# Optimization experiments

Measured on AMD Instinct MI355X. Metric: run time of the kernel, lower is better.

The kernel has to match this reference:

```python
import jax, jax.numpy as jnp
import numpy as np

K = 20
EPS = 1e-5
NEG_SLOPE = 0.2


def _graph_feature(x, k):
    # x: [B, N, C] -> edge features [B, N, k, 2C]
    xx = jnp.sum(x * x, axis=-1)                       # [B, N]
    inner = jnp.einsum('bnc,bmc->bnm', x, x)           # [B, N, N]
    neg_dist = 2.0 * inner - xx[:, :, None] - xx[:, None, :]
    idx = jax.lax.top_k(neg_dist, k)[1]                # [B, N, k] nearest neighbors
    nbr = jax.vmap(lambda f, i: f[i])(x, idx)          # [B, N, k, C]
    center = jnp.broadcast_to(x[:, :, None, :], nbr.shape)
    return jnp.concatenate([nbr - center, center], axis=-1)


def _bn(y, gamma, beta, axes):
    mu = y.mean(axes, keepdims=True)
    var = y.var(axes, keepdims=True)
    return (y - mu) * jax.lax.rsqrt(var + EPS) * gamma + beta


def _lrelu(y):
    return jnp.where(y > 0, y, NEG_SLOPE * y)


def _edge_block(feat, w, gamma, beta):
    # feat: [B, N, k, Cin], w: [Cout, Cin] (1x1 conv)
    y = jnp.einsum('bnkc,oc->bnko', feat, w)
    y = _lrelu(_bn(y, gamma, beta, (0, 1, 2)))
    return y.max(axis=2)                               # max over k -> [B, N, Cout]


def setup_inputs() -> dict:
    key = jax.random.key(0)
    ks = jax.random.split(key, 8)
    B, N = 16, 2048
    num_features = 128
    x = jax.random.normal(ks[0], (B, N, 3), dtype=jnp.float32)
    s = 0.05
    w1 = jax.random.normal(ks[1], (64, 6), dtype=jnp.float32) * s
    w2 = jax.random.normal(ks[2], (64, 128), dtype=jnp.float32) * s
    w3 = jax.random.normal(ks[3], (128, 128), dtype=jnp.float32) * s
    w4 = jax.random.normal(ks[4], (256, 256), dtype=jnp.float32) * s
    w5 = jax.random.normal(ks[5], (512, 512), dtype=jnp.float32) * s
    we = jax.random.normal(ks[6], (num_features, 512), dtype=jnp.float32) * s
    def gb(c):
        return jnp.ones((c,), jnp.float32), jnp.zeros((c,), jnp.float32)
    g1, b1 = gb(64); g2, b2 = gb(64); g3, b3 = gb(128); g4, b4 = gb(256); g5, b5 = gb(512)
    return dict(x=x, w1=w1, g1=g1, b1=b1, w2=w2, g2=g2, b2=b2, w3=w3, g3=g3, b3=b3,
                w4=w4, g4=g4, b4=b4, w5=w5, g5=g5, b5=b5, we=we)


def reference(x, w1, g1, b1, w2, g2, b2, w3, g3, b3, w4, g4, b4, w5, g5, b5, we):
    # x: [B, N, 3]
    x1 = _edge_block(_graph_feature(x, K), w1, g1, b1)    # [B, N, 64]
    x2 = _edge_block(_graph_feature(x1, K), w2, g2, b2)   # [B, N, 64]
    x3 = _edge_block(_graph_feature(x2, K), w3, g3, b3)   # [B, N, 128]
    x4 = _edge_block(_graph_feature(x3, K), w4, g4, b4)   # [B, N, 256]
    cat = jnp.concatenate([x1, x2, x3, x4], axis=-1)      # [B, N, 512]
    y = jnp.einsum('bnc,oc->bno', cat, w5)                # conv5 (1x1 conv1d)
    y = _lrelu(_bn(y, g5, b5, (0, 1)))
    y = y.max(axis=1)                                     # global max pool -> [B, 512]
    return y @ we.T                                       # embedding -> [B, num_features]
```

## Files before the change

### kernel.cpp

```cpp
#include <hip/hip_runtime.h>
#include <hip/hip_bf16.h>
#include <cstdint>

#define B_ 16
#define N_ 2048
#define KNN_K 20
#define EPS_ 1e-5f
#define SLOPE_ 0.2f
#define IMS 4.8828125e-4f

typedef __attribute__((ext_vector_type(4))) float f32x4;
typedef __attribute__((ext_vector_type(8))) short bf16x8;
typedef __attribute__((ext_vector_type(8))) _Float16 f16x8;

static __device__ __forceinline__ float lrelu(float v){ return v > 0.f ? v : SLOPE_*v; }

static __device__ __forceinline__ unsigned encf(float f){
  unsigned b = __float_as_uint(f);
  return (b & 0x80000000u) ? ~b : (b | 0x80000000u);
}
static __device__ __forceinline__ float decf(unsigned u){
  unsigned b = (u & 0x80000000u) ? (u ^ 0x80000000u) : ~u;
  return __uint_as_float(b);
}
static __device__ __forceinline__ short bfbits(float v){
  __hip_bfloat16 h = __float2bfloat16(v);
  return *reinterpret_cast<short*>(&h);
}
static __device__ __forceinline__ short h16(float v){
  _Float16 h = (_Float16)v;
  return *reinterpret_cast<short*>(&h);
}
static __device__ __forceinline__ float h2f(short s){
  _Float16 h = *reinterpret_cast<_Float16*>(&s);
  return (float)h;
}

template<int C, int CP>
__global__ __launch_bounds__(256) void convert_kernel(const float* __restrict__ f, int lda,
                                                      short* __restrict__ fbf, size_t plane,
                                                      float* __restrict__ xx){
  int wid  = (blockIdx.x * 256 + threadIdx.x) >> 6;
  int lane = threadIdx.x & 63;
  if (wid >= B_*N_) return;
  const float* p = f + (size_t)wid*lda;
  float s = 0.f;
  for (int c = lane; c < CP; c += 64){
    float v = (c < C) ? p[c] : 0.f;
    short h = h16(v);
    short m = h16((v - h2f(h)) * 2048.f);
    size_t o = (size_t)wid*CP + c;
    fbf[o] = h;
    fbf[plane + o] = m;
    s += v*v;
  }
  #pragma unroll
  for (int off=32; off; off>>=1) s += __shfl_down(s, off);
  if (lane==0) xx[wid] = s;
}

template<int CP>
__global__ __launch_bounds__(256, 4) void knn_mfma(const short* __restrict__ fbf, size_t plane,
                                                const float* __restrict__ xx,
                                                float* __restrict__ pval, int* __restrict__ pidx){
  constexpr int SP = CP + 8;
  constexpr int CH = CP/8;
  constexpr int KC = CP/32;
  constexpr int PF = CP/16;
  constexpr int FMBS = 2*64*SP;
  constexpr bool ALIAS = (FMBS*2 >= 64*65*4);
  constexpr unsigned LDSB = ALIAS ? (unsigned)(FMBS*2) : (unsigned)(FMBS*2 + 64*65*4);
  __shared__ __align__(16) char ldsbuf[LDSB];
  short* fmb = (short*)ldsbuf;
  float* dtile = ALIAS ? (float*)ldsbuf : (float*)(ldsbuf + FMBS*2);
  __shared__ float xn_s[64], xm_s[64];

  int b   = blockIdx.x >> 6;
  int rem = blockIdx.x & 63;
  int n0  = (rem >> 1) << 6;
  int mh  = rem & 1;
  int mbase = mh << 10;
  int tid = threadIdx.x;
  int w    = tid >> 6;
  int lane = tid & 63;
  int fr = lane & 15, hi = lane >> 4;
  int r_loc = lane >> 2, csub = lane & 3;
  int gb = lane & 60;
  int myrow = w*16 + r_loc;
  size_t browoff = (size_t)b * N_;

  f16x8 aH[KC], aM[KC];
  {
    size_t arow = (browoff + n0 + w*16 + fr) * (size_t)CP;
    #pragma unroll
    for (int kc=0; kc<KC; ++kc){
      aH[kc] = *(const f16x8*)&fbf[arow + kc*32 + hi*8];
      aM[kc] = *(const f16x8*)&fbf[plane + arow + kc*32 + hi*8];
    }
  }
  if (tid < 64) xn_s[tid] = xx[browoff + n0 + tid];

  float sv[5]; int si[5];
  #pragma unroll
  for (int j=0;j<5;++j){ sv[j] = -1e30f; si[j] = 0x7FFFFFFF; }

  f16x8 pf[PF];
  float xmreg = 0.f;
  auto PFLOAD = [&](int mt){
    int m0 = mbase + (mt<<6);
    #pragma unroll
    for (int j=0;j<PF;++j){
      int i = tid + j*256;
      int p = i/(64*CH); int rm = i - p*64*CH; int r = rm/CH, cq = rm - r*CH;
      pf[j] = *(const f16x8*)&fbf[(size_t)p*plane + (browoff + m0 + r)*(size_t)CP + cq*8];
    }
    if (tid < 64) xmreg = xx[browoff + m0 + tid];
  };
  auto WRITEPF = [&](){
    #pragma unroll
    for (int j=0;j<PF;++j){
      int i = tid + j*256;
      int p = i/(64*CH); int rm = i - p*64*CH; int r = rm/CH, cq = rm - r*CH;
      *(f16x8*)&fmb[p*64*SP + r*SP + cq*8] = pf[j];
    }
    if (tid < 64) xm_s[tid] = xmreg;
  };

  PFLOAD(0);
  WRITEPF();
  __syncthreads();

  for (int mt = 0; mt < 16; ++mt){
    int m0 = mbase + (mt << 6);
    if (mt + 1 < 16) PFLOAD(mt + 1);

    f32x4 accH[4], accM[4];
    #pragma unroll
    for (int ct=0; ct<4; ++ct){ accH[ct] = (f32x4){0.f,0.f,0.f,0.f}; accM[ct] = accH[ct]; }
    const short* BH = fmb;
    const short* BM = fmb + 64*SP;
    #pragma unroll
    for (int kc = 0; kc < KC; ++kc){
      #pragma unroll
      for (int ct=0; ct<4; ++ct){
        int boff = (ct*16 + fr)*SP + kc*32 + hi*8;
        f16x8 bh = *(const f16x8*)&BH[boff];
        f16x8 bm = *(const f16x8*)&BM[boff];
        accH[ct] = __builtin_amdgcn_mfma_f32_16x16x32_f16(aH[kc], bh, accH[ct], 0,0,0);
        accM[ct] = __builtin_amdgcn_mfma_f32_16x16x32_f16(aM[kc], bh, accM[ct], 0,0,0);
        accM[ct] = __builtin_amdgcn_mfma_f32_16x16x32_f16(aH[kc], bm, accM[ct], 0,0,0);
      }
    }
    __syncthreads();

    #pragma unroll
    for (int reg=0; reg<4; ++reg){
      int nl = w*16 + hi*4 + reg;
      float xn = xn_s[nl];
      #pragma unroll
      for (int ct=0; ct<4; ++ct)
        dtile[nl*65 + ct*16 + fr] = 2.f*(accH[ct][reg] + IMS*accM[ct][reg]) - xn - xm_s[ct*16 + fr];
    }

    int base = myrow*65 + csub*16;
    float thr = __shfl(sv[4], lane | 3);
    unsigned qm = 0u;
    #pragma unroll
    for (int jj=0; jj<16; ++jj){
      float v = dtile[base + jj];
      qm |= (v > thr) ? (1u << jj) : 0u;
    }
    unsigned long long bal = __ballot(qm != 0u);
    while (bal){
      unsigned nib = (unsigned)((bal >> gb) & 0xFull);
      int leader = nib ? (gb + (int)__builtin_ctz(nib)) : 64;
      int bbit = (int)__builtin_ctz(qm | 0x10000u);
      float mv = dtile[base + (bbit & 15)];
      int mid = m0 + (csub << 4) + bbit;
      float cv = __shfl(mv, leader);
      int   cid = __shfl(mid, leader);
      qm = (lane == leader) ? (qm & (qm - 1u)) : qm;
      int cnt = 0;
      #pragma unroll
      for (int j=0;j<5;++j) cnt += (sv[j] >= cv) ? 1 : 0;
      cnt += __shfl_xor(cnt, 1);
      cnt += __shfl_xor(cnt, 2);
      int pos = nib ? cnt : 20;
      float pv = __shfl_up(sv[4], 1);
      int   pi = __shfl_up(si[4], 1);
      #pragma unroll
      for (int j=0;j<5;++j){
        int g = csub*5 + j;
        float ns = (g < pos) ? sv[j] : ((g == pos) ? cv : pv);
        int   ni = (g < pos) ? si[j] : ((g == pos) ? cid : pi);
        pv = sv[j]; pi = si[j];
        sv[j] = ns; si[j] = ni;
      }
      bal = __ballot(qm != 0u);
    }

    if (mt + 1 < 16){
      if constexpr (ALIAS){
        __syncthreads();
        WRITEPF();
        __syncthreads();
      } else {
        WRITEPF();
        __syncthreads();
      }
    }
  }

  size_t orow = browoff + n0 + myrow;
  float* pvo = pval + (orow*2 + mh)*KNN_K + csub*5;
  int*   pio = pidx + (orow*2 + mh)*KNN_K + csub*5;
  #pragma unroll
  for (int j=0;j<5;++j){ pvo[j] = sv[j]; pio[j] = si[j]; }
}

__global__ __launch_bounds__(256) void knn_merge(const float* __restrict__ pval,
                                                 const int* __restrict__ pidx,
                                                 int* __restrict__ idxout){
  int r = blockIdx.x*256 + threadIdx.x;
  if (r >= B_*N_) return;
  const float* va = pval + (size_t)r*2*KNN_K;
  const float* vb = va + KNN_K;
  const int*   ia = pidx + (size_t)r*2*KNN_K;
  const int*   ib = ia + KNN_K;
  int i=0, j=0;
  #pragma unroll
  for (int t=0;t<KNN_K;++t){
    float a = va[i], bq = vb[j];
    bool ta = (a >= bq);
    idxout[(size_t)r*KNN_K + t] = ta ? ia[i] : ib[j];
    i += ta ? 1 : 0; j += ta ? 0 : 1;
  }
}

template<int CP>
__global__ __launch_bounds__(256) void gemm_pq(const short* __restrict__ fbf, size_t plane,
                                               const float* __restrict__ Wsrc, int wstride, int Cin,
                                               float* __restrict__ Out, int O){
  constexpr int BK = (CP < 64) ? CP : 64;
  constexpr int SP = BK + 8;
  __shared__ short Ah[128*SP];
  __shared__ short Am[128*SP];
  __shared__ short Wh[64*SP];
  __shared__ short Wm[64*SP];
  int obl = O >> 6;
  int bo = ((int)blockIdx.x % obl) << 6;
  int bm = ((int)blockIdx.x / obl) << 7;
  int tid = threadIdx.x;
  int w = tid >> 6, lane = tid & 63;
  int fr = lane & 15, hi = lane >> 4;
  f32x4 accH[2][4], accM[2][4];
  #pragma unroll
  for (int g=0; g<2; ++g)
    #pragma unroll
    for (int ct=0; ct<4; ++ct){ accH[g][ct] = (f32x4){0.f,0.f,0.f,0.f}; accM[g][ct] = accH[g][ct]; }

  for (int k0=0; k0<CP; k0+=BK){
    __syncthreads();
    for (int i=tid; i < 128*(BK/8); i += 256){
      int r = i/(BK/8), cq = i%(BK/8);
      size_t src = ((size_t)bm + r)*CP + k0 + cq*8;
      *(f16x8*)&Ah[r*SP + cq*8] = *(const f16x8*)&fbf[src];
      *(f16x8*)&Am[r*SP + cq*8] = *(const f16x8*)&fbf[plane + src];
    }
    for (int i=tid; i < 64*(BK/8); i += 256){
      int r = i/(BK/8), cq = i%(BK/8);
      f16x8 vh, vm;
      #pragma unroll
      for (int e=0;e<8;++e){
        int c = k0 + cq*8 + e;
        float v = (c < Cin) ? Wsrc[(size_t)(bo + r)*wstride + c] : 0.f;
        _Float16 h = (_Float16)v;
        vh[e] = h;
        vm[e] = (_Float16)((v - (float)h) * 2048.f);
      }
      *(f16x8*)&Wh[r*SP + cq*8] = vh;
      *(f16x8*)&Wm[r*SP + cq*8] = vm;
    }
    __syncthreads();
    #pragma unroll
    for (int kc=0; kc<BK/32; ++kc){
      f16x8 a0h = *(const f16x8*)&Ah[(w*32 +      fr)*SP + kc*32 + hi*8];
      f16x8 a0m = *(const f16x8*)&Am[(w*32 +      fr)*SP + kc*32 + hi*8];
      f16x8 a1h = *(const f16x8*)&Ah[(w*32 + 16 + fr)*SP + kc*32 + hi*8];
      f16x8 a1m = *(const f16x8*)&Am[(w*32 + 16 + fr)*SP + kc*32 + hi*8];
      #pragma unroll
      for (int ct=0; ct<4; ++ct){
        f16x8 bh = *(const f16x8*)&Wh[(ct*16 + fr)*SP + kc*32 + hi*8];
        f16x8 bm = *(const f16x8*)&Wm[(ct*16 + fr)*SP + kc*32 + hi*8];
        accH[0][ct] = __builtin_amdgcn_mfma_f32_16x16x32_f16(a0h, bh, accH[0][ct], 0,0,0);
        accM[0][ct] = __builtin_amdgcn_mfma_f32_16x16x32_f16(a0m, bh, accM[0][ct], 0,0,0);
        accM[0][ct] = __builtin_amdgcn_mfma_f32_16x16x32_f16(a0h, bm, accM[0][ct], 0,0,0);
        accH[1][ct] = __builtin_amdgcn_mfma_f32_16x16x32_f16(a1h, bh, accH[1][ct], 0,0,0);
        accM[1][ct] = __builtin_amdgcn_mfma_f32_16x16x32_f16(a1m, bh, accM[1][ct], 0,0,0);
        accM[1][ct] = __builtin_amdgcn_mfma_f32_16x16x32_f16(a1h, bm, accM[1][ct], 0,0,0);
      }
    }
  }
  #pragma unroll
  for (int g=0; g<2; ++g)
    #pragma unroll
    for (int ct=0; ct<4; ++ct)
      #pragma unroll
      for (int reg=0; reg<4; ++reg){
        int row = bm + w*32 + g*16 + hi*4 + reg;
        Out[(size_t)row*O + bo + ct*16 + fr] = accH[g][ct][reg] + IMS*accM[g][ct][reg];
      }
}

__global__ __launch_bounds__(256) void gemm_bf16(const float* __restrict__ A,
                                                 const float* __restrict__ Wt,
                                                 float* __restrict__ C){
  __shared__ short As[128*72];
  __shared__ short Bs[64*72];
  int bm = (int)(blockIdx.x >> 3) << 7;
  int bo = (int)(blockIdx.x & 7) << 6;
  int tid = threadIdx.x;
  int w = tid >> 6, lane = tid & 63;
  int fr = lane & 15, hi = lane >> 4;
  f32x4 acc[2][4];
  #pragma unroll
  for (int g=0; g<2; ++g)
    #pragma unroll
    for (int ct=0; ct<4; ++ct) acc[g][ct] = (f32x4){0.f,0.f,0.f,0.f};

  for (int k0=0; k0<512; k0+=64){
    __syncthreads();
    #pragma unroll 2
    for (int i = tid; i < 1024; i += 256){
      int r = i >> 3, cq = i & 7;
      const float* src = &A[(size_t)(bm + r)*512 + k0 + cq*8];
      bf16x8 v;
      #pragma unroll
      for (int e=0;e<8;++e) v[e] = bfbits(src[e]);
      *(bf16x8*)&As[r*72 + cq*8] = v;
    }
    #pragma unroll 2
    for (int i = tid; i < 512; i += 256){
      int r = i >> 3, cq = i & 7;
      const float* src = &Wt[(size_t)(bo + r)*512 + k0 + cq*8];
      bf16x8 v;
      #pragma unroll
      for (int e=0;e<8;++e) v[e] = bfbits(src[e]);
      *(bf16x8*)&Bs[r*72 + cq*8] = v;
    }
    __syncthreads();
    #pragma unroll
    for (int kc=0; kc<2; ++kc){
      bf16x8 a0 = *(const bf16x8*)&As[(w*32 +      fr)*72 + kc*32 + hi*8];
      bf16x8 a1 = *(const bf16x8*)&As[(w*32 + 16 + fr)*72 + kc*32 + hi*8];
      #pragma unroll
      for (int ct=0; ct<4; ++ct){
        bf16x8 bb = *(const bf16x8*)&Bs[(ct*16 + fr)*72 + kc*32 + hi*8];
        acc[0][ct] = __builtin_amdgcn_mfma_f32_16x16x32_bf16(a0, bb, acc[0][ct], 0,0,0);
        acc[1][ct] = __builtin_amdgcn_mfma_f32_16x16x32_bf16(a1, bb, acc[1][ct], 0,0,0);
      }
    }
  }
  #pragma unroll
  for (int g=0; g<2; ++g)
    #pragma unroll
    for (int ct=0; ct<4; ++ct)
      #pragma unroll
      for (int reg=0; reg<4; ++reg){
        int row = bm + w*32 + g*16 + hi*4 + reg;
        C[(size_t)row*512 + bo + ct*16 + fr] = acc[g][ct][reg];
      }
}

__global__ void wq_kernel(const float* __restrict__ w, float* __restrict__ wq, int Cin, int O){
  int i = blockIdx.x*blockDim.x + threadIdx.x;
  if (i >= O*Cin) return;
  int o = i / Cin, c = i - o*Cin;
  wq[i] = w[(size_t)o*2*Cin + Cin + c] - w[(size_t)o*2*Cin + c];
}

__global__ void zero_f_kernel(float* p, int n){
  int i = blockIdx.x*blockDim.x + threadIdx.x;
  if (i < n) p[i] = 0.f;
}
__global__ void zero_u_kernel(unsigned* p, int n){
  int i = blockIdx.x*blockDim.x + threadIdx.x;
  if (i < n) p[i] = 0u;
}

__global__ __launch_bounds__(256) void edge_agg(const float* __restrict__ P, const float* __restrict__ Q,
      const int* __restrict__ idx, const float* __restrict__ gamma,
      float* __restrict__ S, float* __restrict__ sums, float* __restrict__ sumsq, int O){
  const int ROWS = 64;
  int rpi = 256 / O;
  int iters = ROWS / rpi;
  int row0 = blockIdx.x * ROWS;
  int tid = threadIdx.x;
  int o  = tid % O;
  int rl = tid / O;
  int b  = row0 / N_;
  __shared__ int sidx[4][KNN_K];
  __shared__ float s1[256], s2[256];
  float g = gamma[o];
  float csum=0.f, csumsq=0.f;
  for (int it=0; it<iters; ++it){
    __syncthreads();
    if (tid < KNN_K*rpi) sidx[tid/KNN_K][tid%KNN_K] = idx[(size_t)(row0 + it*rpi)*KNN_K + tid];
    __syncthreads();
    int row = row0 + it*rpi + rl;
    float q = Q[(size_t)row*O + o];
    float mx=-1e30f, mn=1e30f, s=0.f, ss=0.f;
    #pragma unroll
    for (int k=0;k<KNN_K;++k){
      int m = sidx[rl][k];
      float p = P[((size_t)b*N_ + m)*O + o];
      mx = fmaxf(mx,p); mn = fminf(mn,p);
      float y = p + q; s += y; ss += y*y;
    }
    csum += s; csumsq += ss;
    S[(size_t)row*O + o] = (g >= 0.f ? mx : mn) + q;
  }
  s1[tid]=0.f; s2[tid]=0.f;
  __syncthreads();
  atomicAdd(&s1[o], csum); atomicAdd(&s2[o], csumsq);
  __syncthreads();
  if (tid < O){ atomicAdd(&sums[tid], s1[tid]); atomicAdd(&sumsq[tid], s2[tid]); }
}

__global__ void bn_finalize(const float* __restrict__ sums, const float* __restrict__ sumsq,
                            const float* __restrict__ gamma, const float* __restrict__ beta,
                            float invM, float* __restrict__ scale, float* __restrict__ shift, int O){
  int o = blockIdx.x*blockDim.x + threadIdx.x;
  if (o >= O) return;
  float mu = sums[o]*invM;
  float var = sumsq[o]*invM - mu*mu;
  float rs = rsqrtf(var + EPS_);
  float sc = gamma[o]*rs;
  scale[o] = sc; shift[o] = beta[o] - mu*sc;
}

__global__ void apply_write(const float* __restrict__ S, const float* __restrict__ scale,
                            const float* __restrict__ shift, float* __restrict__ cat, int off, int O){
  int i = blockIdx.x*blockDim.x + threadIdx.x;
  if (i >= B_*N_*O) return;
  int row = i / O, o = i - row*O;
  float v = S[i]*scale[o] + shift[o];
  cat[(size_t)row*512 + off + o] = lrelu(v);
}

__global__ __launch_bounds__(256) void conv5_stats(const float* __restrict__ Y, const float* __restrict__ g5,
      float* __restrict__ sums, float* __restrict__ sumsq, unsigned* __restrict__ maxenc){
  int bb = blockIdx.x / 16;
  int n0 = (blockIdx.x % 16) * 128;
  int tid = threadIdx.x;
  float s0=0.f, s1=0.f, q0=0.f, q1=0.f, m0=-1e30f, m1=-1e30f;
  float ga = g5[tid], gb = g5[tid+256];
  for (int n=0;n<128;++n){
    size_t base = ((size_t)bb*N_ + n0 + n)*512;
    float ya = Y[base + tid];
    float yb = Y[base + tid + 256];
    s0 += ya; q0 += ya*ya;
    s1 += yb; q1 += yb*yb;
    m0 = fmaxf(m0, ga>=0.f ? ya : -ya);
    m1 = fmaxf(m1, gb>=0.f ? yb : -yb);
  }
  atomicAdd(&sums[tid],      s0); atomicAdd(&sumsq[tid],      q0);
  atomicAdd(&sums[tid+256],  s1); atomicAdd(&sumsq[tid+256],  q1);
  atomicMax(&maxenc[bb*512 + tid],       encf(m0));
  atomicMax(&maxenc[bb*512 + tid + 256], encf(m1));
}

__global__ void pool_kernel(const unsigned* __restrict__ maxenc, const float* __restrict__ scale,
                            const float* __restrict__ shift, const float* __restrict__ g5,
                            float* __restrict__ pooled){
  int i = blockIdx.x*blockDim.x + threadIdx.x;
  if (i >= B_*512) return;
  int o = i & 511;
  float t = decf(maxenc[i]);
  float y = g5[o] >= 0.f ? t : -t;
  pooled[i] = lrelu(y*scale[o] + shift[o]);
}

__global__ void final_mm(const float* __restrict__ pooled, const float* __restrict__ we,
                         float* __restrict__ out){
  int i = blockIdx.x*blockDim.x + threadIdx.x;
  if (i >= B_*128) return;
  int b = i >> 7, j = i & 127;
  const float4* pp = (const float4*)(pooled + (size_t)b*512);
  const float4* wp = (const float4*)(we + (size_t)j*512);
  float s = 0.f;
  for (int c=0;c<128;++c){
    float4 a = pp[c], w = wp[c];
    s += a.x*w.x + a.y*w.y + a.z*w.z + a.w*w.w;
  }
  out[i] = s;
}

struct Ws {
  float* cat; float* P; float* Q; float* S; int* idx; float* xx;
  float* sums; float* sumsq; float* scale; float* shift;
  float* wq; unsigned* maxenc; float* pooled; short* fbf;
  float* pval; int* pidx;
};

template<int C, int CP>
static void run_layer(const Ws& W, const float* f, int lda, int O,
                      const float* w, const float* g, const float* bt,
                      int off_out, hipStream_t stream){
  const int M = B_*N_;
  size_t plane = (size_t)M*CP;
  convert_kernel<C, CP><<<M/4, 256, 0, stream>>>(f, lda, W.fbf, plane, W.xx);
  knn_mfma<CP><<<B_*(N_/64)*2, 256, 0, stream>>>(W.fbf, plane, W.xx, W.pval, W.pidx);
  knn_merge<<<(M+255)/256, 256, 0, stream>>>(W.pval, W.pidx, W.idx);
  int nwq = O*C;
  wq_kernel<<<(nwq+255)/256, 256, 0, stream>>>(w, W.wq, C, O);
  int grid = (M/128)*(O/64);
  gemm_pq<CP><<<grid, 256, 0, stream>>>(W.fbf, plane, w,    2*C, C, W.P, O);
  gemm_pq<CP><<<grid, 256, 0, stream>>>(W.fbf, plane, W.wq, C,   C, W.Q, O);
  zero_f_kernel<<<4, 256, 0, stream>>>(W.sums, 1024);
  edge_agg<<<M/64, 256, 0, stream>>>(W.P, W.Q, W.idx, g, W.S, W.sums, W.sumsq, O);
  bn_finalize<<<(O+255)/256, 256, 0, stream>>>(W.sums, W.sumsq, g, bt,
                                               1.f/((float)M*KNN_K), W.scale, W.shift, O);
  apply_write<<<(M*O+255)/256, 256, 0, stream>>>(W.S, W.scale, W.shift, W.cat, off_out, O);
}

extern "C" void kernel_launch(void* const* d_in, const int* in_sizes, int n_in,
                              void* d_out, int out_size, void* d_ws, size_t ws_size,
                              hipStream_t stream) {
  const float* x  = (const float*)d_in[0];
  const float* w1 = (const float*)d_in[1];
  const float* g1 = (const float*)d_in[2];
  const float* b1 = (const float*)d_in[3];
  const float* w2 = (const float*)d_in[4];
  const float* g2 = (const float*)d_in[5];
  const float* b2 = (const float*)d_in[6];
  const float* w3 = (const float*)d_in[7];
  const float* g3 = (const float*)d_in[8];
  const float* b3 = (const float*)d_in[9];
  const float* w4 = (const float*)d_in[10];
  const float* g4 = (const float*)d_in[11];
  const float* b4 = (const float*)d_in[12];
  const float* w5 = (const float*)d_in[13];
  const float* g5 = (const float*)d_in[14];
  const float* b5 = (const float*)d_in[15];
  const float* we = (const float*)d_in[16];

  char* ws = (char*)d_ws;
  Ws W;
  size_t off = 0;
  W.cat   = (float*)(ws + off); off += (size_t)16*2048*512*4;
  W.P     = (float*)(ws + off); off += (size_t)16*2048*256*4;
  W.Q     = (float*)(ws + off); off += (size_t)16*2048*256*4;
  W.S     = (float*)(ws + off); off += (size_t)16*2048*256*4;
  W.idx   = (int*)  (ws + off); off += (size_t)16*2048*20*4;
  W.xx    = (float*)(ws + off); off += (size_t)16*2048*4;
  W.sums  = (float*)(ws + off); off += 512*4;
  W.sumsq = (float*)(ws + off); off += 512*4;
  W.scale = (float*)(ws + off); off += 512*4;
  W.shift = (float*)(ws + off); off += 512*4;
  W.wq    = (float*)(ws + off); off += (size_t)256*128*4;
  W.maxenc= (unsigned*)(ws + off); off += (size_t)16*512*4;
  W.pooled= (float*)(ws + off); off += (size_t)16*512*4;
  W.fbf   = (short*)W.S;
  W.pval  = W.Q;
  W.pidx  = (int*)(W.Q + (size_t)2*16*2048*KNN_K);

  const int M = B_*N_;

  run_layer<3,   32>(W, x,           3,   64,  w1, g1, b1, 0,   stream);
  run_layer<64,  64>(W, W.cat,       512, 64,  w2, g2, b2, 64,  stream);
  run_layer<64,  64>(W, W.cat + 64,  512, 128, w3, g3, b3, 128, stream);
  run_layer<128,128>(W, W.cat + 128, 512, 256, w4, g4, b4, 256, stream);

  float* y5 = W.P;
  gemm_bf16<<<(M/128)*8, 256, 0, stream>>>(W.cat, w5, y5);
  zero_f_kernel<<<4, 256, 0, stream>>>(W.sums, 1024);
  zero_u_kernel<<<32, 256, 0, stream>>>(W.maxenc, 16*512);
  conv5_stats<<<B_*16, 256, 0, stream>>>(y5, g5, W.sums, W.sumsq, W.maxenc);
  bn_finalize<<<2, 256, 0, stream>>>(W.sums, W.sumsq, g5, b5, 1.f/(float)M, W.scale, W.shift, 512);
  pool_kernel<<<(16*512+255)/256, 256, 0, stream>>>(W.maxenc, W.scale, W.shift, g5, W.pooled);
  final_mm<<<(16*128+255)/256, 256, 0, stream>>>(W.pooled, we, (float*)d_out);
}
```

Measured before the change: 1.201 ms.

## Replace LDS-tiled KNN kernel with single-wave blocks loading B directly from global

```diff
diff --git a/kernel.cpp b/kernel.cpp
--- a/kernel.cpp
+++ b/kernel.cpp
@@ -60,109 +60,65 @@
 }
 
 template<int CP>
-__global__ __launch_bounds__(256, 4) void knn_mfma(const short* __restrict__ fbf, size_t plane,
-                                                const float* __restrict__ xx,
-                                                float* __restrict__ pval, int* __restrict__ pidx){
-  constexpr int SP = CP + 8;
-  constexpr int CH = CP/8;
+__global__ __launch_bounds__(64) void knn_nb(const short* __restrict__ fbf, size_t plane,
+                                             const float* __restrict__ xx,
+                                             float* __restrict__ pval, int* __restrict__ pidx){
   constexpr int KC = CP/32;
-  constexpr int PF = CP/16;
-  constexpr int FMBS = 2*64*SP;
-  constexpr bool ALIAS = (FMBS*2 >= 64*65*4);
-  constexpr unsigned LDSB = ALIAS ? (unsigned)(FMBS*2) : (unsigned)(FMBS*2 + 64*65*4);
-  __shared__ __align__(16) char ldsbuf[LDSB];
-  short* fmb = (short*)ldsbuf;
-  float* dtile = ALIAS ? (float*)ldsbuf : (float*)(ldsbuf + FMBS*2);
-  __shared__ float xn_s[64], xm_s[64];
-
-  int b   = blockIdx.x >> 6;
-  int rem = blockIdx.x & 63;
-  int n0  = (rem >> 1) << 6;
-  int mh  = rem & 1;
+  __shared__ float dtile[16*65];
+
+  int b    = blockIdx.x >> 8;
+  int rem  = blockIdx.x & 255;
+  int nblk = rem >> 1;
+  int mh   = rem & 1;
   int mbase = mh << 10;
-  int tid = threadIdx.x;
-  int w    = tid >> 6;
-  int lane = tid & 63;
+  int lane = threadIdx.x;
   int fr = lane & 15, hi = lane >> 4;
   int r_loc = lane >> 2, csub = lane & 3;
   int gb = lane & 60;
-  int myrow = w*16 + r_loc;
+  int n0 = nblk << 4;
   size_t browoff = (size_t)b * N_;
 
   f16x8 aH[KC], aM[KC];
   {
-    size_t arow = (browoff + n0 + w*16 + fr) * (size_t)CP;
+    size_t arow = (browoff + n0 + fr) * (size_t)CP;
     #pragma unroll
     for (int kc=0; kc<KC; ++kc){
       aH[kc] = *(const f16x8*)&fbf[arow + kc*32 + hi*8];
       aM[kc] = *(const f16x8*)&fbf[plane + arow + kc*32 + hi*8];
     }
   }
-  if (tid < 64) xn_s[tid] = xx[browoff + n0 + tid];
 
   float sv[5]; int si[5];
   #pragma unroll
   for (int j=0;j<5;++j){ sv[j] = -1e30f; si[j] = 0x7FFFFFFF; }
-
-  f16x8 pf[PF];
-  float xmreg = 0.f;
-  auto PFLOAD = [&](int mt){
-    int m0 = mbase + (mt<<6);
-    #pragma unroll
-    for (int j=0;j<PF;++j){
-      int i = tid + j*256;
-      int p = i/(64*CH); int rm = i - p*64*CH; int r = rm/CH, cq = rm - r*CH;
-      pf[j] = *(const f16x8*)&fbf[(size_t)p*plane + (browoff + m0 + r)*(size_t)CP + cq*8];
-    }
-    if (tid < 64) xmreg = xx[browoff + m0 + tid];
-  };
-  auto WRITEPF = [&](){
-    #pragma unroll
-    for (int j=0;j<PF;++j){
-      int i = tid + j*256;
-      int p = i/(64*CH); int rm = i - p*64*CH; int r = rm/CH, cq = rm - r*CH;
-      *(f16x8*)&fmb[p*64*SP + r*SP + cq*8] = pf[j];
-    }
-    if (tid < 64) xm_s[tid] = xmreg;
-  };
-
-  PFLOAD(0);
-  WRITEPF();
-  __syncthreads();
 
   for (int mt = 0; mt < 16; ++mt){
     int m0 = mbase + (mt << 6);
-    if (mt + 1 < 16) PFLOAD(mt + 1);
-
-    f32x4 accH[4], accM[4];
-    #pragma unroll
-    for (int ct=0; ct<4; ++ct){ accH[ct] = (f32x4){0.f,0.f,0.f,0.f}; accM[ct] = accH[ct]; }
-    const short* BH = fmb;
-    const short* BM = fmb + 64*SP;
-    #pragma unroll
-    for (int kc = 0; kc < KC; ++kc){
-      #pragma unroll
-      for (int ct=0; ct<4; ++ct){
-        int boff = (ct*16 + fr)*SP + kc*32 + hi*8;
-        f16x8 bh = *(const f16x8*)&BH[boff];
-        f16x8 bm = *(const f16x8*)&BM[boff];
-        accH[ct] = __builtin_amdgcn_mfma_f32_16x16x32_f16(aH[kc], bh, accH[ct], 0,0,0);
-        accM[ct] = __builtin_amdgcn_mfma_f32_16x16x32_f16(aM[kc], bh, accM[ct], 0,0,0);
-        accM[ct] = __builtin_amdgcn_mfma_f32_16x16x32_f16(aH[kc], bm, accM[ct], 0,0,0);
-      }
-    }
-    __syncthreads();
-
-    #pragma unroll
-    for (int reg=0; reg<4; ++reg){
-      int nl = w*16 + hi*4 + reg;
-      float xn = xn_s[nl];
-      #pragma unroll
-      for (int ct=0; ct<4; ++ct)
-        dtile[nl*65 + ct*16 + fr] = 2.f*(accH[ct][reg] + IMS*accM[ct][reg]) - xn - xm_s[ct*16 + fr];
-    }
-
-    int base = myrow*65 + csub*16;
+
+    #pragma unroll
+    for (int ct=0; ct<4; ++ct){
+      const short* bb = fbf + (browoff + m0 + ct*16 + fr)*(size_t)CP + hi*8;
+      f16x8 bh[KC], bm[KC];
+      #pragma unroll
+      for (int kc=0; kc<KC; ++kc){
+        bh[kc] = *(const f16x8*)(bb + kc*32);
+        bm[kc] = *(const f16x8*)(bb + plane + kc*32);
+      }
+      f32x4 accH = (f32x4){0.f,0.f,0.f,0.f};
+      f32x4 accM = accH;
+      #pragma unroll
+      for (int kc=0; kc<KC; ++kc){
+        accH = __builtin_amdgcn_mfma_f32_16x16x32_f16(aH[kc], bh[kc], accH, 0,0,0);
+        accM = __builtin_amdgcn_mfma_f32_16x16x32_f16(aM[kc], bh[kc], accM, 0,0,0);
+        accM = __builtin_amdgcn_mfma_f32_16x16x32_f16(aH[kc], bm[kc], accM, 0,0,0);
+      }
+      float xm = xx[browoff + m0 + ct*16 + fr];
+      #pragma unroll
+      for (int reg=0; reg<4; ++reg)
+        dtile[(hi*4+reg)*65 + ct*16 + fr] = 2.f*(accH[reg] + IMS*accM[reg]) - xm;
+    }
+
+    int base = r_loc*65 + csub*16;
     float thr = __shfl(sv[4], lane | 3);
     unsigned qm = 0u;
     #pragma unroll
@@ -198,20 +154,9 @@
       }
       bal = __ballot(qm != 0u);
     }
-
-    if (mt + 1 < 16){
-      if constexpr (ALIAS){
-        __syncthreads();
-        WRITEPF();
-        __syncthreads();
-      } else {
-        WRITEPF();
-        __syncthreads();
-      }
-    }
-  }
-
-  size_t orow = browoff + n0 + myrow;
+  }
+
+  size_t orow = browoff + n0 + r_loc;
   float* pvo = pval + (orow*2 + mh)*KNN_K + csub*5;
   int*   pio = pidx + (orow*2 + mh)*KNN_K + csub*5;
   #pragma unroll
@@ -510,7 +455,7 @@
   const int M = B_*N_;
   size_t plane = (size_t)M*CP;
   convert_kernel<C, CP><<<M/4, 256, 0, stream>>>(f, lda, W.fbf, plane, W.xx);
-  knn_mfma<CP><<<B_*(N_/64)*2, 256, 0, stream>>>(W.fbf, plane, W.xx, W.pval, W.pidx);
+  knn_nb<CP><<<B_*(N_/16)*2, 64, 0, stream>>>(W.fbf, plane, W.xx, W.pval, W.pidx);
   knn_merge<<<(M+255)/256, 256, 0, stream>>>(W.pval, W.pidx, W.idx);
   int nwq = O*C;
   wq_kernel<<<(nwq+255)/256, 256, 0, stream>>>(w, W.wq, C, O);
```

New measurement: 1.304 ms. +8.6%, slower.
